# Performance work log

Measured on AMD Instinct MI355X. Metric: run time of the kernel, lower is better.

The kernel has to match this reference:

```python
import jax, jax.numpy as jnp
import numpy as np

D, H, HS, L, V, B, T = 384, 8, 48, 8, 32000, 32, 128
EPS = 1e-5


def setup_inputs() -> dict:
    key = jax.random.key(0)
    ks = jax.random.split(key, 10)
    s = 0.02
    return {
        'index': jax.random.randint(ks[0], (B, T), 0, V),
        'tok_emb': jax.random.normal(ks[1], (V, D), jnp.float32) * s,
        'pos_emb': jax.random.normal(ks[2], (V, D), jnp.float32) * s,
        'Wq': jax.random.normal(ks[3], (L, D, D), jnp.float32) * s,
        'Wk': jax.random.normal(ks[4], (L, D, D), jnp.float32) * s,
        'Wv': jax.random.normal(ks[5], (L, D, D), jnp.float32) * s,
        'Wo': jax.random.normal(ks[6], (L, D, D), jnp.float32) * s,
        'bo': jnp.zeros((L, D), jnp.float32),
        'W1': jax.random.normal(ks[7], (L, D, 4 * D), jnp.float32) * s,
        'b1': jnp.zeros((L, 4 * D), jnp.float32),
        'W2': jax.random.normal(ks[8], (L, 4 * D, D), jnp.float32) * s,
        'b2': jnp.zeros((L, D), jnp.float32),
        'ln1g': jnp.ones((L, D), jnp.float32),
        'ln1b': jnp.zeros((L, D), jnp.float32),
        'ln2g': jnp.ones((L, D), jnp.float32),
        'ln2b': jnp.zeros((L, D), jnp.float32),
        'lnfg': jnp.ones((D,), jnp.float32),
        'lnfb': jnp.zeros((D,), jnp.float32),
        'lmW': jax.random.normal(ks[9], (D, V), jnp.float32) * s,
        'lmb': jnp.zeros((V,), jnp.float32),
    }


def _layer_norm(x, g, b):
    m = jnp.mean(x, axis=-1, keepdims=True)
    xc = x - m
    v = jnp.mean(xc * xc, axis=-1, keepdims=True)
    return xc * jax.lax.rsqrt(v + EPS) * g + b


def _forward(index, tok_emb, pos_emb, Wq, Wk, Wv, Wo, bo, W1, b1, W2, b2,
             ln1g, ln1b, ln2g, ln2b, lnfg, lnfb, lmW, lmb):
    Bx, Tx = index.shape
    x = tok_emb[index] + pos_emb[jnp.arange(Tx)]  # [B,T,D]
    tril = jnp.tril(jnp.ones((Tx, Tx), bool))
    scale = HS ** -0.5
    neg_inf = jnp.finfo(x.dtype).min
    for l in range(L):
        q = (x @ Wq[l]).reshape(Bx, Tx, H, HS)
        k = (x @ Wk[l]).reshape(Bx, Tx, H, HS)
        v = (x @ Wv[l]).reshape(Bx, Tx, H, HS)
        wei = jnp.einsum('bthd,bshd->bhts', q, k) * scale  # [B,H,T,T]
        wei = jnp.where(tril, wei, neg_inf)
        wei = jax.nn.softmax(wei, axis=-1)
        attn = jnp.einsum('bhts,bshd->bthd', wei, v).reshape(Bx, Tx, D)
        y = attn @ Wo[l] + bo[l]
        x = _layer_norm(x + y, ln1g[l], ln1b[l])  # post-LN as in source
        y = jax.nn.relu(x @ W1[l] + b1[l]) @ W2[l] + b2[l]
        x = _layer_norm(x + y, ln2g[l], ln2b[l])
    x = _layer_norm(x, lnfg, lnfb)
    logits = x @ lmW + lmb  # [B,T,V]
    return logits


def reference(index, tok_emb, pos_emb, Wq, Wk, Wv, Wo, bo, W1, b1, W2, b2,
              ln1g, ln1b, ln2g, ln2b, lnfg, lnfb, lmW, lmb):
    return _forward(index, tok_emb, pos_emb, Wq, Wk, Wv, Wo, bo, W1, b1, W2,
                    b2, ln1g, ln1b, ln2g, ln2b, lnfg, lnfb, lmW, lmb)
```

## Files before the change

kernel.cpp:

```cpp
#include <hip/hip_runtime.h>
#include <cstdint>
#include <cstddef>

#define D_  384
#define H_  8
#define HS_ 48
#define L_  8
#define V_  32000
#define B_  32
#define T_  128
#define M_  4096

typedef __bf16 bf16;
typedef __bf16 bf16x8 __attribute__((ext_vector_type(8)));
typedef float  floatx4 __attribute__((ext_vector_type(4)));

__device__ __forceinline__ unsigned short bfbits(float f) {
  union { bf16 b; unsigned short u; } cv; cv.b = (bf16)f; return cv.u;
}
__device__ __forceinline__ float bflo(unsigned u) {
  union { float f; unsigned x; } c; c.x = u << 16; return c.f;
}
__device__ __forceinline__ float bfhi(unsigned u) {
  union { float f; unsigned x; } c; c.x = u & 0xffff0000u; return c.f;
}

__device__ __forceinline__ float waveReduceSum(float v) {
  #pragma unroll
  for (int off = 32; off > 0; off >>= 1) v += __shfl_xor(v, off, 64);
  return v;
}

__device__ __forceinline__ void gload_lds16(const void* g, void* l) {
  __builtin_amdgcn_global_load_lds(
      (const __attribute__((address_space(1))) void*)g,
      (__attribute__((address_space(3))) void*)l, 16, 0, 0);
}

__global__ void embed_kernel(const int* __restrict__ idx, const float* __restrict__ tok,
                             const float* __restrict__ pos, float* __restrict__ x,
                             bf16* __restrict__ xb) {
  int e = blockIdx.x * 256 + threadIdx.x;
  int row = e / 96, c4 = (e % 96) * 4;
  int t = row & (T_ - 1);
  int tk = idx[row];
  const float4 tv = *(const float4*)(tok + (size_t)tk * D_ + c4);
  const float4 pv = *(const float4*)(pos + (size_t)t * D_ + c4);
  float4 o; o.x = tv.x + pv.x; o.y = tv.y + pv.y; o.z = tv.z + pv.z; o.w = tv.w + pv.w;
  *(float4*)(x + (size_t)row * D_ + c4) = o;
  uint2 u;
  u.x = (unsigned)bfbits(o.x) | ((unsigned)bfbits(o.y) << 16);
  u.y = (unsigned)bfbits(o.z) | ((unsigned)bfbits(o.w) << 16);
  *(uint2*)(xb + (size_t)row * D_ + c4) = u;
}

__device__ __forceinline__ void transpose_tile(const float* __restrict__ src, bf16* __restrict__ dst,
                                               int K, int N, int k0, int n0) {
  __shared__ float tile[32][33];
  const int r = threadIdx.x >> 5, c = threadIdx.x & 31;
  #pragma unroll
  for (int i = 0; i < 4; i++)
    tile[r + 8*i][c] = src[(size_t)(k0 + r + 8*i) * N + n0 + c];
  __syncthreads();
  #pragma unroll
  for (int i = 0; i < 4; i++)
    dst[(size_t)(n0 + r + 8*i) * K + k0 + c] = (bf16)tile[c][r + 8*i];
}

__global__ __launch_bounds__(256) void t_layer_kernel(
    const float* __restrict__ Wq, const float* __restrict__ Wk,
    const float* __restrict__ Wv, const float* __restrict__ Wo,
    const float* __restrict__ W1, const float* __restrict__ W2,
    bf16* __restrict__ wqkvoT, bf16* __restrict__ w1t, bf16* __restrict__ w2t) {
  if (blockIdx.z == 0) {
    const int mm = blockIdx.x / 12, nx = blockIdx.x % 12;
    const float* src = mm == 0 ? Wq : mm == 1 ? Wk : mm == 2 ? Wv : Wo;
    transpose_tile(src, wqkvoT + (size_t)mm * (D_ * D_), D_, D_, blockIdx.y * 32, nx * 32);
  } else if (blockIdx.z == 1) {
    transpose_tile(W1, w1t, D_, 4 * D_, blockIdx.y * 32, blockIdx.x * 32);
  } else {
    transpose_tile(W2, w2t, 4 * D_, D_, blockIdx.x * 32, blockIdx.y * 32);
  }
}

__global__ __launch_bounds__(256) void t_head_kernel(const float* __restrict__ lmW, bf16* __restrict__ dst) {
  transpose_tile(lmW, dst, D_, V_, blockIdx.y * 32, blockIdx.x * 32);
}

template<int BM, bool BIAS, bool RESID, bool RELU, bool OUTBF>
__device__ __forceinline__ void gemm_core(
    const bf16* __restrict__ A, const bf16* __restrict__ Bt,
    const float* __restrict__ bias, const float* __restrict__ resid,
    void* __restrict__ Cout, int N, int K, int m0, int n0)
{
  constexpr int MTC = BM / 32;
  __shared__ bf16 As[2][BM * 32];
  __shared__ bf16 Bs[2][128 * 32];
  const int tid  = threadIdx.x;
  const int lane = tid & 63;
  const int wave = tid >> 6;
  const int wr = wave >> 1, wc = wave & 1;
  const int lrow = lane & 15, quad = lane >> 4;
  const int rdoff = ((quad ^ ((lrow >> 1) & 3)) << 3);

  const int srow = lane >> 2;
  const int scol = (((lane & 3) ^ ((lane >> 3) & 3)) << 3);

  floatx4 acc[MTC][4];
  #pragma unroll
  for (int i = 0; i < MTC; i++)
    #pragma unroll
    for (int j = 0; j < 4; j++) acc[i][j] = floatx4{0.f, 0.f, 0.f, 0.f};

  const bf16* gA = A  + (size_t)(m0 + wave * (BM / 4) + srow) * K + scol;
  const bf16* gB = Bt + (size_t)(n0 + wave * 32       + srow) * K + scol;

  auto STAGE = [&](int buf, int kk) {
    bf16* lA = &As[buf][wave * (BM * 8)];
    bf16* lB = &Bs[buf][wave * 1024];
    #pragma unroll
    for (int j = 0; j < BM / 64; j++)
      gload_lds16(gA + kk + (size_t)j * 16 * K, lA + j * 512);
    #pragma unroll
    for (int j = 0; j < 2; j++)
      gload_lds16(gB + kk + (size_t)j * 16 * K, lB + j * 512);
  };

  STAGE(0, 0);
  __syncthreads();
  int cur = 0;
  for (int k0 = 0; k0 < K; k0 += 32) {
    if (k0 + 32 < K) STAGE(cur ^ 1, k0 + 32);
    bf16x8 af[MTC], bfr[4];
    #pragma unroll
    for (int mt = 0; mt < MTC; mt++)
      af[mt]  = *(const bf16x8*)&As[cur][(wr * (BM / 2) + mt * 16 + lrow) * 32 + rdoff];
    #pragma unroll
    for (int nt = 0; nt < 4; nt++)
      bfr[nt] = *(const bf16x8*)&Bs[cur][(wc * 64 + nt * 16 + lrow) * 32 + rdoff];
    #pragma unroll
    for (int mt = 0; mt < MTC; mt++)
      #pragma unroll
      for (int nt = 0; nt < 4; nt++)
        acc[mt][nt] = __builtin_amdgcn_mfma_f32_16x16x32_bf16(af[mt], bfr[nt], acc[mt][nt], 0, 0, 0);
    __syncthreads();
    cur ^= 1;
  }

  #pragma unroll
  for (int mt = 0; mt < MTC; mt++) {
    #pragma unroll
    for (int nt = 0; nt < 4; nt++) {
      const int col = n0 + wc * 64 + nt * 16 + lrow;
      float bv = 0.f;
      if (BIAS) bv = bias[col];
      #pragma unroll
      for (int i = 0; i < 4; i++) {
        const int row = m0 + wr * (BM / 2) + mt * 16 + quad * 4 + i;
        float vv = acc[mt][nt][i] + bv;
        if (RESID) vv += resid[(size_t)row * N + col];
        if (RELU)  vv = vv > 0.f ? vv : 0.f;
        if (OUTBF) ((bf16*)Cout)[(size_t)row * N + col] = (bf16)vv;
        else       ((float*)Cout)[(size_t)row * N + col] = vv;
      }
    }
  }
}

template<int BM, bool BIAS, bool RESID, bool RELU, bool OUTBF>
__global__ __launch_bounds__(256) void gemm_kernel(const bf16* __restrict__ A, const bf16* __restrict__ Bt,
    const float* __restrict__ bias, const float* __restrict__ resid, void* __restrict__ C, int N, int K) {
  gemm_core<BM, BIAS, RESID, RELU, OUTBF>(A, Bt, bias, resid, C, N, K, blockIdx.x * BM, blockIdx.y * 128);
}

__global__ __launch_bounds__(256) void gemm_qkv_kernel(const bf16* __restrict__ A, const bf16* __restrict__ Wt,
    bf16* __restrict__ q, bf16* __restrict__ k, bf16* __restrict__ v) {
  const bf16* Bt = Wt + (size_t)blockIdx.z * (D_ * D_);
  bf16* C = blockIdx.z == 0 ? q : (blockIdx.z == 1 ? k : v);
  gemm_core<128, false, false, false, true>(A, Bt, nullptr, nullptr, C, D_, D_, blockIdx.x * 128, blockIdx.y * 128);
}

__global__ __launch_bounds__(512) void attn_kernel(const bf16* __restrict__ q,
    const bf16* __restrict__ k, const bf16* __restrict__ v, bf16* __restrict__ attnb) {
  __shared__ float ks[T_][48];
  __shared__ float vs[T_][48];
  const int bh = blockIdx.x;
  const int b = bh >> 3, h = bh & 7;
  const int r  = threadIdx.x >> 2;
  const int qq = threadIdx.x & 3;
  const int o  = qq * 12;
  const size_t rowbase = ((size_t)(b * T_ + r)) * D_ + h * HS_ + o;
  float qr[12];
  #pragma unroll
  for (int j = 0; j < 3; j++) {
    const uint2 tk = *(const uint2*)(k + rowbase + 4*j);
    const uint2 tv = *(const uint2*)(v + rowbase + 4*j);
    const uint2 tq = *(const uint2*)(q + rowbase + 4*j);
    float4 fk, fv;
    fk.x = bflo(tk.x); fk.y = bfhi(tk.x); fk.z = bflo(tk.y); fk.w = bfhi(tk.y);
    fv.x = bflo(tv.x); fv.y = bfhi(tv.x); fv.z = bflo(tv.y); fv.w = bfhi(tv.y);
    *(float4*)&ks[r][o + 4*j] = fk;
    *(float4*)&vs[r][o + 4*j] = fv;
    qr[4*j]   = bflo(tq.x); qr[4*j+1] = bfhi(tq.x);
    qr[4*j+2] = bflo(tq.y); qr[4*j+3] = bfhi(tq.y);
  }
  __syncthreads();
  float m = -3.0e38f, l = 0.f, acc[12];
  #pragma unroll
  for (int j = 0; j < 12; j++) acc[j] = 0.f;
  const float scale = 0.14433756729740643f;
  for (int c = 0; c < T_; c++) {
    float s = 0.f;
    #pragma unroll
    for (int j = 0; j < 12; j++) s += qr[j] * ks[c][o + j];
    s += __shfl_xor(s, 1, 64);
    s += __shfl_xor(s, 2, 64);
    s *= scale;
    if (c > r) s = -3.0e38f;
    const float mn = fmaxf(m, s);
    const float al = __expf(m - mn);
    const float pp = __expf(s - mn);
    l = l * al + pp;
    #pragma unroll
    for (int j = 0; j < 12; j++) acc[j] = acc[j] * al + pp * vs[c][o + j];
    m = mn;
  }
  const float inv = 1.f / l;
  unsigned ob[6];
  #pragma unroll
  for (int j = 0; j < 6; j++)
    ob[j] = (unsigned)bfbits(acc[2*j] * inv) | ((unsigned)bfbits(acc[2*j+1] * inv) << 16);
  bf16* dst = attnb + rowbase;
  #pragma unroll
  for (int j = 0; j < 3; j++) {
    uint2 u; u.x = ob[2*j]; u.y = ob[2*j+1];
    *(uint2*)(dst + 4*j) = u;
  }
}

__global__ __launch_bounds__(256) void ln_kernel(const float* __restrict__ in,
    const float* __restrict__ g, const float* __restrict__ bta,
    float* __restrict__ xo, bf16* __restrict__ xbo) {
  const int wave = threadIdx.x >> 6, lane = threadIdx.x & 63;
  const int row = blockIdx.x * 4 + wave;
  const float* p = in + (size_t)row * D_;
  float v[6];
  #pragma unroll
  for (int j = 0; j < 6; j++) v[j] = p[lane + 64*j];
  float s = 0.f;
  #pragma unroll
  for (int j = 0; j < 6; j++) s += v[j];
  s = waveReduceSum(s);
  const float mean = s * (1.f / 384.f);
  float qv = 0.f;
  #pragma unroll
  for (int j = 0; j < 6; j++) { v[j] -= mean; qv += v[j] * v[j]; }
  qv = waveReduceSum(qv);
  const float rs = rsqrtf(qv * (1.f / 384.f) + 1e-5f);
  #pragma unroll
  for (int j = 0; j < 6; j++) {
    const int c = lane + 64*j;
    const float o = v[j] * rs * g[c] + bta[c];
    xo[(size_t)row * D_ + c]  = o;
    xbo[(size_t)row * D_ + c] = (bf16)o;
  }
}

extern "C" void kernel_launch(void* const* d_in, const int* in_sizes, int n_in,
                              void* d_out, int out_size, void* d_ws, size_t ws_size,
                              hipStream_t stream) {
  const int*   index = (const int*)  d_in[0];
  const float* tok   = (const float*)d_in[1];
  const float* pos   = (const float*)d_in[2];
  const float* Wq    = (const float*)d_in[3];
  const float* Wk    = (const float*)d_in[4];
  const float* Wv    = (const float*)d_in[5];
  const float* Wo    = (const float*)d_in[6];
  const float* bo    = (const float*)d_in[7];
  const float* W1    = (const float*)d_in[8];
  const float* b1    = (const float*)d_in[9];
  const float* W2    = (const float*)d_in[10];
  const float* b2    = (const float*)d_in[11];
  const float* ln1g  = (const float*)d_in[12];
  const float* ln1b  = (const float*)d_in[13];
  const float* ln2g  = (const float*)d_in[14];
  const float* ln2b  = (const float*)d_in[15];
  const float* lnfg  = (const float*)d_in[16];
  const float* lnfb  = (const float*)d_in[17];
  const float* lmW   = (const float*)d_in[18];
  const float* lmb   = (const float*)d_in[19];
  float* out = (float*)d_out;
  char* ws = (char*)d_ws;

  float* x     = (float*)(ws + 0);
  float* tmp   = (float*)(ws + 6291456);
  bf16*  xb    = (bf16*) (ws + 12582912);
  bf16*  qb    = (bf16*) (ws + 15728640);
  bf16*  kb    = (bf16*) (ws + 18874368);
  bf16*  vb    = (bf16*) (ws + 22020096);
  bf16*  attnb = (bf16*) (ws + 25165824);
  bf16*  hb    = (bf16*) (ws + 28311552);
  bf16*  wqkvoT= (bf16*) (ws + 40894464);
  bf16*  w1t   = (bf16*) (ws + 42074112);
  bf16*  w2t   = (bf16*) (ws + 43253760);
  bf16*  lmT   = (bf16*) (ws + 15728640);

  embed_kernel<<<1536, 256, 0, stream>>>(index, tok, pos, x, xb);
  for (int l = 0; l < L_; l++) {
    t_layer_kernel<<<dim3(48, 12, 3), 256, 0, stream>>>(
        Wq + (size_t)l * D_ * D_, Wk + (size_t)l * D_ * D_,
        Wv + (size_t)l * D_ * D_, Wo + (size_t)l * D_ * D_,
        W1 + (size_t)l * D_ * 4 * D_, W2 + (size_t)l * 4 * D_ * D_,
        wqkvoT, w1t, w2t);
    gemm_qkv_kernel<<<dim3(32, 3, 3), 256, 0, stream>>>(xb, wqkvoT, qb, kb, vb);
    attn_kernel<<<256, 512, 0, stream>>>(qb, kb, vb, attnb);
    gemm_kernel<64, true, true, false, false><<<dim3(64, 3), 256, 0, stream>>>(
        attnb, wqkvoT + 3 * D_ * D_, bo + l * D_, x, tmp, D_, D_);
    ln_kernel<<<1024, 256, 0, stream>>>(tmp, ln1g + l * D_, ln1b + l * D_, x, xb);
    gemm_kernel<128, true, false, true, true><<<dim3(32, 12), 256, 0, stream>>>(
        xb, w1t, b1 + l * 4 * D_, nullptr, hb, 4 * D_, D_);
    gemm_kernel<64, true, true, false, false><<<dim3(64, 3), 256, 0, stream>>>(
        hb, w2t, b2 + l * D_, x, tmp, D_, 4 * D_);
    ln_kernel<<<1024, 256, 0, stream>>>(tmp, ln2g + l * D_, ln2b + l * D_, x, xb);
  }
  ln_kernel<<<1024, 256, 0, stream>>>(x, lnfg, lnfb, x, xb);
  t_head_kernel<<<dim3(1000, 12), 256, 0, stream>>>(lmW, lmT);
  gemm_kernel<128, true, false, false, false><<<dim3(32, 250), 256, 0, stream>>>(
      xb, lmT, lmb, nullptr, out, V_, D_);
}
```

Measured before the change: 1.635 ms.

## Fuse residual LayerNorm into projection GEMMs and overlap next-layer weight transpose with FFN1

Adds a gemm_ln_kernel where each block computes 16 full rows of the 384-wide output. Bias, residual add and LayerNorm are applied in the epilogue, so the fp32 tmp round-trip and the separate ln_kernel launches go away. Weight transposition for layer l+1 is folded into the FFN1 GEMM launch via extra grid z-slices, writing into double-buffered weight buffers. This removes per-layer launches and a serial transpose phase, but the fused GEMM uses only 256 blocks with small M tiles and single-pass variance, which may lower MFMA efficiency and precision.

```diff
diff --git a/kernel.cpp b/kernel.cpp
--- a/kernel.cpp
+++ b/kernel.cpp
@@ -178,6 +178,129 @@
   const bf16* Bt = Wt + (size_t)blockIdx.z * (D_ * D_);
   bf16* C = blockIdx.z == 0 ? q : (blockIdx.z == 1 ? k : v);
   gemm_core<128, false, false, false, true>(A, Bt, nullptr, nullptr, C, D_, D_, blockIdx.x * 128, blockIdx.y * 128);
+}
+
+__global__ __launch_bounds__(256) void ffn1t_kernel(
+    const bf16* __restrict__ A, const bf16* __restrict__ Bt, const float* __restrict__ bias,
+    bf16* __restrict__ hb,
+    const float* __restrict__ nWq, const float* __restrict__ nWk,
+    const float* __restrict__ nWv, const float* __restrict__ nWo,
+    const float* __restrict__ nW1, const float* __restrict__ nW2,
+    bf16* __restrict__ nwqkvoT, bf16* __restrict__ nw1t, bf16* __restrict__ nw2t) {
+  if (blockIdx.z == 0) {
+    if (blockIdx.x >= 32) return;
+    gemm_core<128, true, false, true, true>(A, Bt, bias, nullptr, hb, 4 * D_, D_,
+                                            blockIdx.x * 128, blockIdx.y * 128);
+  } else if (blockIdx.z == 1) {
+    const int mm = blockIdx.x / 12, nx = blockIdx.x % 12;
+    const float* src = mm == 0 ? nWq : mm == 1 ? nWk : mm == 2 ? nWv : nWo;
+    transpose_tile(src, nwqkvoT + (size_t)mm * (D_ * D_), D_, D_, blockIdx.y * 32, nx * 32);
+  } else if (blockIdx.z == 2) {
+    transpose_tile(nW1, nw1t, D_, 4 * D_, blockIdx.y * 32, blockIdx.x * 32);
+  } else {
+    transpose_tile(nW2, nw2t, 4 * D_, D_, blockIdx.x * 32, blockIdx.y * 32);
+  }
+}
+
+__global__ __launch_bounds__(256) void gemm_ln_kernel(
+    const bf16* __restrict__ A, const bf16* __restrict__ Bt,
+    const float* __restrict__ bias, const float* __restrict__ g,
+    const float* __restrict__ beta, float* __restrict__ x,
+    bf16* __restrict__ xb, int K)
+{
+  __shared__ bf16 As[2][16 * 32];
+  __shared__ bf16 Bs[2][384 * 32];
+  __shared__ float red[4][16][2];
+  const int tid  = threadIdx.x;
+  const int lane = tid & 63;
+  const int wave = tid >> 6;
+  const int lrow = lane & 15, quad = lane >> 4;
+  const int m0 = blockIdx.x * 16;
+  const int rdoff = ((quad ^ ((lrow >> 1) & 3)) << 3);
+  const int srow = lane >> 2;
+  const int scol = (((lane & 3) ^ ((lane >> 3) & 3)) << 3);
+
+  floatx4 acc[6];
+  #pragma unroll
+  for (int j = 0; j < 6; j++) acc[j] = floatx4{0.f, 0.f, 0.f, 0.f};
+
+  auto STAGE = [&](int buf, int kk) {
+    #pragma unroll
+    for (int i = 0; i < 6; i++) {
+      const int c = wave * 6 + i;
+      gload_lds16(Bt + (size_t)(c * 16 + srow) * K + kk + scol, &Bs[buf][c * 512]);
+    }
+    if (wave == 0)
+      gload_lds16(A + (size_t)(m0 + srow) * K + kk + scol, &As[buf][0]);
+  };
+
+  STAGE(0, 0);
+  __syncthreads();
+  int cur = 0;
+  for (int k0 = 0; k0 < K; k0 += 32) {
+    if (k0 + 32 < K) STAGE(cur ^ 1, k0 + 32);
+    const bf16x8 af = *(const bf16x8*)&As[cur][lrow * 32 + rdoff];
+    bf16x8 bfr[6];
+    #pragma unroll
+    for (int nt = 0; nt < 6; nt++)
+      bfr[nt] = *(const bf16x8*)&Bs[cur][(wave * 96 + nt * 16 + lrow) * 32 + rdoff];
+    #pragma unroll
+    for (int nt = 0; nt < 6; nt++)
+      acc[nt] = __builtin_amdgcn_mfma_f32_16x16x32_bf16(af, bfr[nt], acc[nt], 0, 0, 0);
+    __syncthreads();
+    cur ^= 1;
+  }
+
+  float sum[4] = {0.f, 0.f, 0.f, 0.f}, sq[4] = {0.f, 0.f, 0.f, 0.f};
+  #pragma unroll
+  for (int nt = 0; nt < 6; nt++) {
+    const int col = wave * 96 + nt * 16 + lrow;
+    const float bv = bias[col];
+    #pragma unroll
+    for (int i = 0; i < 4; i++) {
+      const int row = m0 + quad * 4 + i;
+      const float t = acc[nt][i] + bv + x[(size_t)row * D_ + col];
+      acc[nt][i] = t;
+      sum[i] += t; sq[i] += t * t;
+    }
+  }
+  #pragma unroll
+  for (int off = 1; off <= 8; off <<= 1) {
+    #pragma unroll
+    for (int i = 0; i < 4; i++) {
+      sum[i] += __shfl_xor(sum[i], off, 64);
+      sq[i]  += __shfl_xor(sq[i],  off, 64);
+    }
+  }
+  if (lrow == 0) {
+    #pragma unroll
+    for (int i = 0; i < 4; i++) {
+      red[wave][quad * 4 + i][0] = sum[i];
+      red[wave][quad * 4 + i][1] = sq[i];
+    }
+  }
+  __syncthreads();
+  float mean[4], rs[4];
+  #pragma unroll
+  for (int i = 0; i < 4; i++) {
+    const int rr = quad * 4 + i;
+    const float S = red[0][rr][0] + red[1][rr][0] + red[2][rr][0] + red[3][rr][0];
+    const float Q = red[0][rr][1] + red[1][rr][1] + red[2][rr][1] + red[3][rr][1];
+    mean[i] = S * (1.f / 384.f);
+    rs[i] = rsqrtf(Q * (1.f / 384.f) - mean[i] * mean[i] + 1e-5f);
+  }
+  #pragma unroll
+  for (int nt = 0; nt < 6; nt++) {
+    const int col = wave * 96 + nt * 16 + lrow;
+    const float gv = g[col], bt = beta[col];
+    #pragma unroll
+    for (int i = 0; i < 4; i++) {
+      const int row = m0 + quad * 4 + i;
+      const float o = (acc[nt][i] - mean[i]) * rs[i] * gv + bt;
+      x[(size_t)row * D_ + col]  = o;
+      xb[(size_t)row * D_ + col] = (bf16)o;
+    }
+  }
 }
 
 __global__ __launch_bounds__(512) void attn_kernel(const bf16* __restrict__ q,
@@ -293,35 +416,44 @@
   char* ws = (char*)d_ws;
 
   float* x     = (float*)(ws + 0);
-  float* tmp   = (float*)(ws + 6291456);
-  bf16*  xb    = (bf16*) (ws + 12582912);
-  bf16*  qb    = (bf16*) (ws + 15728640);
-  bf16*  kb    = (bf16*) (ws + 18874368);
-  bf16*  vb    = (bf16*) (ws + 22020096);
-  bf16*  attnb = (bf16*) (ws + 25165824);
-  bf16*  hb    = (bf16*) (ws + 28311552);
-  bf16*  wqkvoT= (bf16*) (ws + 40894464);
-  bf16*  w1t   = (bf16*) (ws + 42074112);
-  bf16*  w2t   = (bf16*) (ws + 43253760);
-  bf16*  lmT   = (bf16*) (ws + 15728640);
+  bf16*  xb    = (bf16*) (ws + 6291456);
+  bf16*  qb    = (bf16*) (ws + 9437184);
+  bf16*  kb    = (bf16*) (ws + 12582912);
+  bf16*  vb    = (bf16*) (ws + 15728640);
+  bf16*  attnb = (bf16*) (ws + 18874368);
+  bf16*  hb    = (bf16*) (ws + 22020096);
+  char*  wbuf0 = ws + 34603008;
+  char*  wbuf1 = ws + 38141952;
+  bf16*  lmT   = (bf16*) (ws + 9437184);
+
+  auto wq_of = [&](char* wb) { return (bf16*)wb; };
+  auto w1_of = [&](char* wb) { return (bf16*)(wb + 1179648); };
+  auto w2_of = [&](char* wb) { return (bf16*)(wb + 2359296); };
 
   embed_kernel<<<1536, 256, 0, stream>>>(index, tok, pos, x, xb);
+  t_layer_kernel<<<dim3(48, 12, 3), 256, 0, stream>>>(
+      Wq, Wk, Wv, Wo, W1, W2, wq_of(wbuf0), w1_of(wbuf0), w2_of(wbuf0));
+
   for (int l = 0; l < L_; l++) {
-    t_layer_kernel<<<dim3(48, 12, 3), 256, 0, stream>>>(
-        Wq + (size_t)l * D_ * D_, Wk + (size_t)l * D_ * D_,
-        Wv + (size_t)l * D_ * D_, Wo + (size_t)l * D_ * D_,
-        W1 + (size_t)l * D_ * 4 * D_, W2 + (size_t)l * 4 * D_ * D_,
-        wqkvoT, w1t, w2t);
-    gemm_qkv_kernel<<<dim3(32, 3, 3), 256, 0, stream>>>(xb, wqkvoT, qb, kb, vb);
+    char* wb  = (l & 1) ? wbuf1 : wbuf0;
+    char* nwb = (l & 1) ? wbuf0 : wbuf1;
+    gemm_qkv_kernel<<<dim3(32, 3, 3), 256, 0, stream>>>(xb, wq_of(wb), qb, kb, vb);
     attn_kernel<<<256, 512, 0, stream>>>(qb, kb, vb, attnb);
-    gemm_kernel<64, true, true, false, false><<<dim3(64, 3), 256, 0, stream>>>(
-        attnb, wqkvoT + 3 * D_ * D_, bo + l * D_, x, tmp, D_, D_);
-    ln_kernel<<<1024, 256, 0, stream>>>(tmp, ln1g + l * D_, ln1b + l * D_, x, xb);
-    gemm_kernel<128, true, false, true, true><<<dim3(32, 12), 256, 0, stream>>>(
-        xb, w1t, b1 + l * 4 * D_, nullptr, hb, 4 * D_, D_);
-    gemm_kernel<64, true, true, false, false><<<dim3(64, 3), 256, 0, stream>>>(
-        hb, w2t, b2 + l * D_, x, tmp, D_, 4 * D_);
-    ln_kernel<<<1024, 256, 0, stream>>>(tmp, ln2g + l * D_, ln2b + l * D_, x, xb);
+    gemm_ln_kernel<<<256, 256, 0, stream>>>(
+        attnb, wq_of(wb) + 3 * D_ * D_, bo + l * D_, ln1g + l * D_, ln1b + l * D_, x, xb, D_);
+    if (l < L_ - 1) {
+      const size_t o1 = (size_t)(l + 1) * D_ * D_;
+      const size_t o2 = (size_t)(l + 1) * D_ * 4 * D_;
+      ffn1t_kernel<<<dim3(48, 12, 4), 256, 0, stream>>>(
+          xb, w1_of(wb), b1 + l * 4 * D_, hb,
+          Wq + o1, Wk + o1, Wv + o1, Wo + o1, W1 + o2, W2 + o2,
+          wq_of(nwb), w1_of(nwb), w2_of(nwb));
+    } else {
+      gemm_kernel<128, true, false, true, true><<<dim3(32, 12), 256, 0, stream>>>(
+          xb, w1_of(wb), b1 + l * 4 * D_, nullptr, hb, 4 * D_, D_);
+    }
+    gemm_ln_kernel<<<256, 256, 0, stream>>>(
+        hb, w2_of(wb), b2 + l * D_, ln2g + l * D_, ln2b + l * D_, x, xb, 4 * D_);
   }
   ln_kernel<<<1024, 256, 0, stream>>>(x, lnfg, lnfb, x, xb);
   t_head_kernel<<<dim3(1000, 12), 256, 0, stream>>>(lmW, lmT);
```

Result: no change. 1.642 ms (+0.4%).
